# Performance work log

Measured on AMD Instinct MI355X. Metric: run time of the kernel, lower is better.

Reference implementation:

```python
import jax, jax.numpy as jnp
import numpy as np

B, TQ, TV, D, UNITS = 4, 256, 256, 512, 512
NEG_INF = -1e9

def setup_inputs() -> dict:
    key = jax.random.key(0)
    ks = jax.random.split(key, 5)
    return {
        "query": jax.random.normal(ks[0], (B, TQ, D), dtype=jnp.float32),
        "value": jax.random.normal(ks[1], (B, TV, D), dtype=jnp.float32),
        "mask": jnp.ones((B, TV), dtype=bool),
        "W1": jax.random.normal(ks[2], (D, UNITS), dtype=jnp.float32) * (1.0 / np.sqrt(D)),
        "W2": jax.random.normal(ks[3], (D, UNITS), dtype=jnp.float32) * (1.0 / np.sqrt(D)),
        "scale": jax.random.normal(ks[4], (UNITS,), dtype=jnp.float32),
    }

def reference(query, value, mask, W1, W2, scale):
    # Dual projections
    q = query @ W1                      # [B,Tq,U]
    k = value @ W2                      # [B,Tv,U]
    # Additive (Bahdanau) scores: sum(scale * tanh(q + k)) over units
    # broadcast tensor [B,Tq,Tv,U] is what the kernel would tile/fuse away
    t = jnp.tanh(q[:, :, None, :] + k[:, None, :, :])   # [B,Tq,Tv,U]
    scores = jnp.einsum('btvu,u->btv', t, scale)         # [B,Tq,Tv]
    # mask over value (key) positions
    scores = jnp.where(mask[:, None, :], scores, NEG_INF)
    attn = jax.nn.softmax(scores, axis=-1)               # [B,Tq,Tv]
    context = jnp.einsum('btv,bvd->btd', attn, value)    # [B,Tq,D]
    return context, attn
```

## Files before the change

### kernel.cpp

```cpp
#include <hip/hip_runtime.h>

typedef float f4 __attribute__((ext_vector_type(4)));
typedef float f2 __attribute__((ext_vector_type(2)));
typedef short short8 __attribute__((ext_vector_type(8)));
typedef float f32x4 __attribute__((ext_vector_type(4)));

#define NEG_INF -1e9f

__device__ inline void bsplit(float x, unsigned short& h, unsigned short& l) {
  union { float f; unsigned u; } a; a.f = x;
  unsigned rh = (a.u + 0x7fffu + ((a.u >> 16) & 1u)) >> 16;
  h = (unsigned short)rh;
  union { unsigned u; float f; } b; b.u = rh << 16;
  union { float f; unsigned u; } c; c.f = x - b.f;
  unsigned rl = (c.u + 0x7fffu + ((c.u >> 16) & 1u)) >> 16;
  l = (unsigned short)rl;
}

__device__ inline void gl_lds16(const void* g, void* l) {
  __builtin_amdgcn_global_load_lds(
      (const __attribute__((address_space(1))) unsigned int*)g,
      (__attribute__((address_space(3))) unsigned int*)l, 16, 0, 0);
}

__global__ __launch_bounds__(256) void conv_aw(
    const float* __restrict__ q, const float* __restrict__ v,
    const float* __restrict__ W1, const float* __restrict__ W2,
    unsigned short* __restrict__ Ahi, unsigned short* __restrict__ Alo,
    unsigned short* __restrict__ Whi, unsigned short* __restrict__ Wlo)
{
  __shared__ float ldsW[128][64];
  const int t = threadIdx.x;

  if (blockIdx.x < 512) {
    const int g = blockIdx.x * 256 + t;
    const int row64 = g & 63;
    const int panel = (g >> 6) & 31;
    const int kc    = g >> 11;
    const int rowg  = panel * 64 + row64;
    const float* src = (rowg < 1024) ? (q + (size_t)rowg * 512 + kc * 8)
                                     : (v + (size_t)(rowg - 1024) * 512 + kc * 8);
    f4 x0 = *reinterpret_cast<const f4*>(src);
    f4 x1 = *reinterpret_cast<const f4*>(src + 4);
    unsigned short h[8], l[8];
#pragma unroll
    for (int j = 0; j < 4; ++j) { bsplit(x0[j], h[j], l[j]); bsplit(x1[j], h[4+j], l[4+j]); }
    const size_t off = ((size_t)(panel * 64 + kc) * 64 + row64) * 8;
    short8 ph, pl;
#pragma unroll
    for (int j = 0; j < 8; ++j) { ph[j] = (short)h[j]; pl[j] = (short)l[j]; }
    *reinterpret_cast<short8*>(&Ahi[off]) = ph;
    *reinterpret_cast<short8*>(&Alo[off]) = pl;
    return;
  }

  const int bid   = blockIdx.x - 512;
  const int kslab = bid & 3;
  const int np    = (bid >> 2) & 7;
  const int z     = bid >> 5;
  const float* __restrict__ W = z ? W2 : W1;
  const int k0 = kslab * 128, n0 = np * 64;

#pragma unroll
  for (int it = 0; it < 8; ++it) {
    const int idx = it * 256 + t;
    const int kr  = idx >> 4;
    const int nc4 = (idx & 15) * 4;
    *reinterpret_cast<f4*>(&ldsW[kr][nc4]) =
        *reinterpret_cast<const f4*>(&W[(size_t)(k0 + kr) * 512 + n0 + nc4]);
  }
  __syncthreads();

  const int wpanel = z * 8 + np;
  const int n = t & 63;
#pragma unroll
  for (int it = 0; it < 4; ++it) {
    const int kcl = it * 4 + (t >> 6);
    short8 ph, pl;
#pragma unroll
    for (int j = 0; j < 8; ++j) {
      unsigned short h, l;
      bsplit(ldsW[kcl * 8 + j][n], h, l);
      ph[j] = (short)h; pl[j] = (short)l;
    }
    const size_t off = ((size_t)(wpanel * 64 + kslab * 16 + kcl) * 64 + n) * 8;
    *reinterpret_cast<short8*>(&Whi[off]) = ph;
    *reinterpret_cast<short8*>(&Wlo[off]) = pl;
  }
}

__global__ __launch_bounds__(256) void projmm(
    const unsigned short* __restrict__ Ahi, const unsigned short* __restrict__ Alo,
    const unsigned short* __restrict__ Whi, const unsigned short* __restrict__ Wlo,
    float* __restrict__ EQ, float* __restrict__ EKT)
{
  const int nb = blockIdx.x, mb = blockIdx.y, z = blockIdx.z;
  const int t = threadIdx.x;
  const int l = t & 63;
  const int w = t >> 6;
  const int wr = w >> 1, wc = w & 1;

  __shared__ __align__(16) short Ast[2][2][2048];
  __shared__ __align__(16) short Bst[2][2][2048];
  __shared__ float ldsT[64][67];

  const unsigned short* abase_h = Ahi + (size_t)(z * 16 + mb) * 32768;
  const unsigned short* abase_l = Alo + (size_t)(z * 16 + mb) * 32768;
  const unsigned short* wbase_h = Whi + (size_t)(z * 8 + nb) * 32768;
  const unsigned short* wbase_l = Wlo + (size_t)(z * 8 + nb) * 32768;

  const int ldst = (t >> 6) * 512;
  const int gsrc = t * 8;

#define STAGE(buf, ks)                                                        \
  do {                                                                        \
    gl_lds16(abase_h + (ks) * 2048 + gsrc, &Ast[buf][0][ldst]);               \
    gl_lds16(abase_l + (ks) * 2048 + gsrc, &Ast[buf][1][ldst]);               \
    gl_lds16(wbase_h + (ks) * 2048 + gsrc, &Bst[buf][0][ldst]);               \
    gl_lds16(wbase_l + (ks) * 2048 + gsrc, &Bst[buf][1][ldst]);               \
  } while (0)

  f32x4 acc[2][2] = {};
  STAGE(0, 0);
  __syncthreads();

  int buf = 0;
  for (int ks = 0; ks < 16; ++ks) {
    if (ks < 15) STAGE(buf ^ 1, ks + 1);
    const int kgo = (l >> 4) * 1024;
    short8 ah[2], al[2], bh[2], bl[2];
#pragma unroll
    for (int i = 0; i < 2; ++i) {
      const int ro = (wr * 32 + i * 16 + (l & 15)) * 16;
      ah[i] = *reinterpret_cast<const short8*>((const char*)&Ast[buf][0][0] + kgo + ro);
      al[i] = *reinterpret_cast<const short8*>((const char*)&Ast[buf][1][0] + kgo + ro);
    }
#pragma unroll
    for (int j = 0; j < 2; ++j) {
      const int co = (wc * 32 + j * 16 + (l & 15)) * 16;
      bh[j] = *reinterpret_cast<const short8*>((const char*)&Bst[buf][0][0] + kgo + co);
      bl[j] = *reinterpret_cast<const short8*>((const char*)&Bst[buf][1][0] + kgo + co);
    }
#pragma unroll
    for (int i = 0; i < 2; ++i)
#pragma unroll
      for (int j = 0; j < 2; ++j) {
        acc[i][j] = __builtin_amdgcn_mfma_f32_16x16x32_bf16(ah[i], bh[j], acc[i][j], 0, 0, 0);
        acc[i][j] = __builtin_amdgcn_mfma_f32_16x16x32_bf16(ah[i], bl[j], acc[i][j], 0, 0, 0);
        acc[i][j] = __builtin_amdgcn_mfma_f32_16x16x32_bf16(al[i], bh[j], acc[i][j], 0, 0, 0);
      }
    __syncthreads();
    buf ^= 1;
  }

  if (z == 0) {
#pragma unroll
    for (int i = 0; i < 2; ++i)
#pragma unroll
      for (int j = 0; j < 2; ++j)
#pragma unroll
        for (int r = 0; r < 4; ++r) {
          const int row = mb * 64 + wr * 32 + i * 16 + (l >> 4) * 4 + r;
          const int col = nb * 64 + wc * 32 + j * 16 + (l & 15);
          EQ[(size_t)row * 512 + col] = __expf(2.0f * acc[i][j][r]);
        }
  } else {
#pragma unroll
    for (int i = 0; i < 2; ++i)
#pragma unroll
      for (int j = 0; j < 2; ++j)
#pragma unroll
        for (int r = 0; r < 4; ++r) {
          const int rl = wr * 32 + i * 16 + (l >> 4) * 4 + r;
          const int cl = wc * 32 + j * 16 + (l & 15);
          ldsT[rl][cl] = __expf(2.0f * acc[i][j][r]);
        }
    __syncthreads();
    const int b  = (mb * 64) >> 8;
    const int v0 = (mb * 64) & 255;
    const int vl = t & 63;
#pragma unroll
    for (int it = 0; it < 16; ++it) {
      const int ul = it * 4 + (t >> 6);
      EKT[(size_t)b * 131072 + (size_t)(nb * 64 + ul) * 256 + v0 + vl] = ldsT[vl][ul];
    }
  }
#undef STAGE
}

__global__ __launch_bounds__(1024) void bah_attn(
    const float* __restrict__ EQ, const float* __restrict__ EKT,
    const float* __restrict__ value, const int* __restrict__ mask,
    const float* __restrict__ scale,
    float* __restrict__ ctx_out, float* __restrict__ attn_out)
{
  const int blk = blockIdx.x;
  const int b  = (blk & 7) >> 1;
  const int tg = (blk >> 3) + ((blk & 1) << 5);
  const int tq0 = tg * 4;
  const int bq  = b * 256 + tq0;

  const int tid = threadIdx.x;
  const int v4  = tid & 63;
  const int uq  = tid >> 6;
  const int w   = tid >> 6;
  const int l   = tid & 63;

  __shared__ f4    eq4s[512];
  __shared__ float ss[512];
  __shared__ float wredM[4][4];
  __shared__ float wredS[4][4];
  __shared__ float sumS_lds;
  __shared__ float atT[256][4];
  __shared__ __align__(16) char uA[131072];
  float* const ubufF = (float*)uA;
  float* const partF = (float*)uA;
  float* const ctxpF = (float*)(uA + 65536);

  const float* __restrict__ ekb = EKT + (size_t)b * (512 * 256);
  const float* __restrict__ eqb = EQ + (size_t)bq * 512;

  const int u0 = uq * 32;
  float* const wbase = ubufF + uq * 2048;

  const int r   = w & 3;
  const int vg  = w >> 2;
  const int v   = vg * 64 + l;

#define STAGEW(bufp, s)                                                       \
  do {                                                                        \
    _Pragma("unroll")                                                         \
    for (int c_ = 0; c_ < 4; ++c_)                                            \
      gl_lds16(ekb + (size_t)(u0 + (s) * 4 + c_) * 256 + l * 4,               \
               wbase + (bufp) * 1024 + c_ * 256);                             \
  } while (0)

  STAGEW(0, 0);

  const bool mok = (mask[b * 256 + v] != 0);

  {
    const int h  = tid >> 9;
    const int u2 = tid & 511;
    f2 e;
    e[0] = eqb[(size_t)(2 * h) * 512 + u2];
    e[1] = eqb[(size_t)(2 * h + 1) * 512 + u2];
    *(reinterpret_cast<f2*>(&eq4s[u2]) + h) = e;
    if (h == 0) ss[u2] = scale[u2];
  }
  __syncthreads();

  if (w == 0) {
    float s = 0.f;
#pragma unroll
    for (int j = 0; j < 8; ++j) s += ss[l + 64 * j];
#pragma unroll
    for (int off = 32; off; off >>= 1) s += __shfl_xor(s, off);
    if (l == 0) sumS_lds = s;
  }

  f2 accp[4][2] = {};
  int bufi = 0;
#pragma unroll 1
  for (int s = 0; s < 8; ++s) {
    if (s < 7) {
      STAGEW(bufi ^ 1, s + 1);
      asm volatile("s_waitcnt vmcnt(4)" ::: "memory");
    } else {
      asm volatile("s_waitcnt vmcnt(0)" ::: "memory");
    }
    __builtin_amdgcn_sched_barrier(0);
    const float* bp = wbase + bufi * 1024;
#pragma unroll
    for (int cp = 0; cp < 2; ++cp) {
      const int uA_ = u0 + s * 4 + 2 * cp;
      const f4 ekA4 = *reinterpret_cast<const f4*>(bp + (2 * cp) * 256 + v4 * 4);
      const f4 ekB4 = *reinterpret_cast<const f4*>(bp + (2 * cp + 1) * 256 + v4 * 4);
      const f2 ekA[2] = {{ekA4[0], ekA4[1]}, {ekA4[2], ekA4[3]}};
      const f2 ekB[2] = {{ekB4[0], ekB4[1]}, {ekB4[2], ekB4[3]}};
      const f4 eqA = eq4s[uA_];
      const f4 eqB = eq4s[uA_ + 1];
      const f2 sp  = *reinterpret_cast<const f2*>(&ss[uA_]);
      const f2 sA2 = {sp[0], sp[0]};
      const f2 sB2 = {sp[1], sp[1]};
      const f2 one2 = {1.0f, 1.0f};
#pragma unroll
      for (int i = 0; i < 4; ++i) {
        const f2 eA2 = {eqA[i], eqA[i]};
        const f2 eB2 = {eqB[i], eqB[i]};
#pragma unroll
        for (int jh = 0; jh < 2; ++jh) {
          const f2 dA  = __builtin_elementwise_fma(eA2, ekA[jh], one2);
          const f2 dB  = __builtin_elementwise_fma(eB2, ekB[jh], one2);
          const f2 num = __builtin_elementwise_fma(sA2, dB, sB2 * dA);
          const f2 P   = dA * dB;
          f2 r_;
          r_[0] = __builtin_amdgcn_rcpf(P[0]);
          r_[1] = __builtin_amdgcn_rcpf(P[1]);
          accp[i][jh] = __builtin_elementwise_fma(num, r_, accp[i][jh]);
        }
      }
    }
    bufi ^= 1;
  }

#pragma unroll
  for (int i = 0; i < 4; ++i) {
    const f4 a4 = {accp[i][0][0], accp[i][0][1], accp[i][1][0], accp[i][1][1]};
    *reinterpret_cast<f4*>(partF + uq * 2048 + i * 256 + v4 * 4) = a4;
  }
  __syncthreads();

  float sc, ex;
  {
    float p = 0.f;
#pragma unroll
    for (int u2 = 0; u2 < 16; ++u2) p += partF[u2 * 2048 + r * 256 + v];
    sc = mok ? (sumS_lds - 2.0f * p) : NEG_INF;
    float m = sc;
#pragma unroll
    for (int off = 32; off; off >>= 1) m = fmaxf(m, __shfl_xor(m, off));
    if (l == 0) wredM[r][vg] = m;
  }
  __syncthreads();

  {
    const float m = fmaxf(fmaxf(wredM[r][0], wredM[r][1]),
                          fmaxf(wredM[r][2], wredM[r][3]));
    ex = __expf(sc - m);
    float sm = ex;
#pragma unroll
    for (int off = 32; off; off >>= 1) sm += __shfl_xor(sm, off);
    if (l == 0) wredS[r][vg] = sm;
  }
  __syncthreads();

  {
    const float denom = (wredS[r][0] + wredS[r][1]) + (wredS[r][2] + wredS[r][3]);
    const float a = ex * __builtin_amdgcn_rcpf(denom);
    atT[v][r] = a;
    attn_out[(size_t)(bq + r) * 256 + v] = a;
  }
  __syncthreads();

  const int vc8 = w & 7;
  const int dh  = w >> 3;
  const float* __restrict__ vb = value + (size_t)b * (256 * 512) + dh * 256;
  f4 g0 = {0,0,0,0}, g1 = {0,0,0,0}, g2 = {0,0,0,0}, g3 = {0,0,0,0};
#pragma unroll 4
  for (int v2 = 0; v2 < 32; ++v2) {
    const int vv = vc8 * 32 + v2;
    const f4 a4 = *reinterpret_cast<const f4*>(&atT[vv][0]);
    const f4 x  = *reinterpret_cast<const f4*>(&vb[(size_t)vv * 512 + l * 4]);
    g0 += a4[0] * x;
    g1 += a4[1] * x;
    g2 += a4[2] * x;
    g3 += a4[3] * x;
  }
  {
    float* const cp = ctxpF + vc8 * 2048 + dh * 256 + l * 4;
    *reinterpret_cast<f4*>(cp + 0 * 512) = g0;
    *reinterpret_cast<f4*>(cp + 1 * 512) = g1;
    *reinterpret_cast<f4*>(cp + 2 * 512) = g2;
    *reinterpret_cast<f4*>(cp + 3 * 512) = g3;
  }
  __syncthreads();

  {
    const int row = tid >> 8;
    const int d2  = (tid & 255) * 2;
    f2 s = {0.f, 0.f};
#pragma unroll
    for (int vc = 0; vc < 8; ++vc)
      s += *reinterpret_cast<const f2*>(ctxpF + vc * 2048 + row * 512 + d2);
    *reinterpret_cast<f2*>(&ctx_out[(size_t)(bq + row) * 512 + d2]) = s;
  }
#undef STAGEW
}

extern "C" void kernel_launch(void* const* d_in, const int* in_sizes, int n_in,
                              void* d_out, int out_size, void* d_ws, size_t ws_size,
                              hipStream_t stream) {
  const float* query = (const float*)d_in[0];
  const float* value = (const float*)d_in[1];
  const int*   mask  = (const int*)d_in[2];
  const float* W1    = (const float*)d_in[3];
  const float* W2    = (const float*)d_in[4];
  const float* scale = (const float*)d_in[5];

  char* ws = (char*)d_ws;
  float* EQ  = (float*)(ws);
  float* EKT = (float*)(ws + (2u << 20));
  unsigned short* Ahi = (unsigned short*)(ws + (4u << 20));
  unsigned short* Alo = (unsigned short*)(ws + (6u << 20));
  unsigned short* Whi = (unsigned short*)(ws + (8u << 20));
  unsigned short* Wlo = (unsigned short*)(ws + (9u << 20));

  float* ctx  = (float*)d_out;
  float* attn = ctx + 4 * 256 * 512;

  conv_aw<<<dim3(576), 256, 0, stream>>>(query, value, W1, W2, Ahi, Alo, Whi, Wlo);
  projmm<<<dim3(8, 16, 2), 256, 0, stream>>>(Ahi, Alo, Whi, Wlo, EQ, EKT);
  bah_attn<<<dim3(256), 1024, 0, stream>>>(EQ, EKT, value, mask, scale, ctx, attn);
}
```

Measured before the change: 46.76 us.

## Fuse conversion, projection and attention into one cooperative kernel with grid syncs

```diff
diff --git a/kernel.cpp b/kernel.cpp
--- a/kernel.cpp
+++ b/kernel.cpp
@@ -1,4 +1,7 @@
 #include <hip/hip_runtime.h>
+#include <hip/hip_cooperative_groups.h>
+
+namespace cg = cooperative_groups;
 
 typedef float f4 __attribute__((ext_vector_type(4)));
 typedef float f2 __attribute__((ext_vector_type(2)));
@@ -23,188 +26,18 @@
       (__attribute__((address_space(3))) unsigned int*)l, 16, 0, 0);
 }
 
-__global__ __launch_bounds__(256) void conv_aw(
-    const float* __restrict__ q, const float* __restrict__ v,
+__global__ __launch_bounds__(1024) void bah_fused(
+    const float* __restrict__ query, const float* __restrict__ value,
+    const int* __restrict__ mask,
     const float* __restrict__ W1, const float* __restrict__ W2,
+    const float* __restrict__ scale,
     unsigned short* __restrict__ Ahi, unsigned short* __restrict__ Alo,
-    unsigned short* __restrict__ Whi, unsigned short* __restrict__ Wlo)
-{
-  __shared__ float ldsW[128][64];
-  const int t = threadIdx.x;
-
-  if (blockIdx.x < 512) {
-    const int g = blockIdx.x * 256 + t;
-    const int row64 = g & 63;
-    const int panel = (g >> 6) & 31;
-    const int kc    = g >> 11;
-    const int rowg  = panel * 64 + row64;
-    const float* src = (rowg < 1024) ? (q + (size_t)rowg * 512 + kc * 8)
-                                     : (v + (size_t)(rowg - 1024) * 512 + kc * 8);
-    f4 x0 = *reinterpret_cast<const f4*>(src);
-    f4 x1 = *reinterpret_cast<const f4*>(src + 4);
-    unsigned short h[8], l[8];
-#pragma unroll
-    for (int j = 0; j < 4; ++j) { bsplit(x0[j], h[j], l[j]); bsplit(x1[j], h[4+j], l[4+j]); }
-    const size_t off = ((size_t)(panel * 64 + kc) * 64 + row64) * 8;
-    short8 ph, pl;
-#pragma unroll
-    for (int j = 0; j < 8; ++j) { ph[j] = (short)h[j]; pl[j] = (short)l[j]; }
-    *reinterpret_cast<short8*>(&Ahi[off]) = ph;
-    *reinterpret_cast<short8*>(&Alo[off]) = pl;
-    return;
-  }
-
-  const int bid   = blockIdx.x - 512;
-  const int kslab = bid & 3;
-  const int np    = (bid >> 2) & 7;
-  const int z     = bid >> 5;
-  const float* __restrict__ W = z ? W2 : W1;
-  const int k0 = kslab * 128, n0 = np * 64;
-
-#pragma unroll
-  for (int it = 0; it < 8; ++it) {
-    const int idx = it * 256 + t;
-    const int kr  = idx >> 4;
-    const int nc4 = (idx & 15) * 4;
-    *reinterpret_cast<f4*>(&ldsW[kr][nc4]) =
-        *reinterpret_cast<const f4*>(&W[(size_t)(k0 + kr) * 512 + n0 + nc4]);
-  }
-  __syncthreads();
-
-  const int wpanel = z * 8 + np;
-  const int n = t & 63;
-#pragma unroll
-  for (int it = 0; it < 4; ++it) {
-    const int kcl = it * 4 + (t >> 6);
-    short8 ph, pl;
-#pragma unroll
-    for (int j = 0; j < 8; ++j) {
-      unsigned short h, l;
-      bsplit(ldsW[kcl * 8 + j][n], h, l);
-      ph[j] = (short)h; pl[j] = (short)l;
-    }
-    const size_t off = ((size_t)(wpanel * 64 + kslab * 16 + kcl) * 64 + n) * 8;
-    *reinterpret_cast<short8*>(&Whi[off]) = ph;
-    *reinterpret_cast<short8*>(&Wlo[off]) = pl;
-  }
-}
-
-__global__ __launch_bounds__(256) void projmm(
-    const unsigned short* __restrict__ Ahi, const unsigned short* __restrict__ Alo,
-    const unsigned short* __restrict__ Whi, const unsigned short* __restrict__ Wlo,
-    float* __restrict__ EQ, float* __restrict__ EKT)
-{
-  const int nb = blockIdx.x, mb = blockIdx.y, z = blockIdx.z;
-  const int t = threadIdx.x;
-  const int l = t & 63;
-  const int w = t >> 6;
-  const int wr = w >> 1, wc = w & 1;
-
-  __shared__ __align__(16) short Ast[2][2][2048];
-  __shared__ __align__(16) short Bst[2][2][2048];
-  __shared__ float ldsT[64][67];
-
-  const unsigned short* abase_h = Ahi + (size_t)(z * 16 + mb) * 32768;
-  const unsigned short* abase_l = Alo + (size_t)(z * 16 + mb) * 32768;
-  const unsigned short* wbase_h = Whi + (size_t)(z * 8 + nb) * 32768;
-  const unsigned short* wbase_l = Wlo + (size_t)(z * 8 + nb) * 32768;
-
-  const int ldst = (t >> 6) * 512;
-  const int gsrc = t * 8;
-
-#define STAGE(buf, ks)                                                        \
-  do {                                                                        \
-    gl_lds16(abase_h + (ks) * 2048 + gsrc, &Ast[buf][0][ldst]);               \
-    gl_lds16(abase_l + (ks) * 2048 + gsrc, &Ast[buf][1][ldst]);               \
-    gl_lds16(wbase_h + (ks) * 2048 + gsrc, &Bst[buf][0][ldst]);               \
-    gl_lds16(wbase_l + (ks) * 2048 + gsrc, &Bst[buf][1][ldst]);               \
-  } while (0)
-
-  f32x4 acc[2][2] = {};
-  STAGE(0, 0);
-  __syncthreads();
-
-  int buf = 0;
-  for (int ks = 0; ks < 16; ++ks) {
-    if (ks < 15) STAGE(buf ^ 1, ks + 1);
-    const int kgo = (l >> 4) * 1024;
-    short8 ah[2], al[2], bh[2], bl[2];
-#pragma unroll
-    for (int i = 0; i < 2; ++i) {
-      const int ro = (wr * 32 + i * 16 + (l & 15)) * 16;
-      ah[i] = *reinterpret_cast<const short8*>((const char*)&Ast[buf][0][0] + kgo + ro);
-      al[i] = *reinterpret_cast<const short8*>((const char*)&Ast[buf][1][0] + kgo + ro);
-    }
-#pragma unroll
-    for (int j = 0; j < 2; ++j) {
-      const int co = (wc * 32 + j * 16 + (l & 15)) * 16;
-      bh[j] = *reinterpret_cast<const short8*>((const char*)&Bst[buf][0][0] + kgo + co);
-      bl[j] = *reinterpret_cast<const short8*>((const char*)&Bst[buf][1][0] + kgo + co);
-    }
-#pragma unroll
-    for (int i = 0; i < 2; ++i)
-#pragma unroll
-      for (int j = 0; j < 2; ++j) {
-        acc[i][j] = __builtin_amdgcn_mfma_f32_16x16x32_bf16(ah[i], bh[j], acc[i][j], 0, 0, 0);
-        acc[i][j] = __builtin_amdgcn_mfma_f32_16x16x32_bf16(ah[i], bl[j], acc[i][j], 0, 0, 0);
-        acc[i][j] = __builtin_amdgcn_mfma_f32_16x16x32_bf16(al[i], bh[j], acc[i][j], 0, 0, 0);
-      }
-    __syncthreads();
-    buf ^= 1;
-  }
-
-  if (z == 0) {
-#pragma unroll
-    for (int i = 0; i < 2; ++i)
-#pragma unroll
-      for (int j = 0; j < 2; ++j)
-#pragma unroll
-        for (int r = 0; r < 4; ++r) {
-          const int row = mb * 64 + wr * 32 + i * 16 + (l >> 4) * 4 + r;
-          const int col = nb * 64 + wc * 32 + j * 16 + (l & 15);
-          EQ[(size_t)row * 512 + col] = __expf(2.0f * acc[i][j][r]);
-        }
-  } else {
-#pragma unroll
-    for (int i = 0; i < 2; ++i)
-#pragma unroll
-      for (int j = 0; j < 2; ++j)
-#pragma unroll
-        for (int r = 0; r < 4; ++r) {
-          const int rl = wr * 32 + i * 16 + (l >> 4) * 4 + r;
-          const int cl = wc * 32 + j * 16 + (l & 15);
-          ldsT[rl][cl] = __expf(2.0f * acc[i][j][r]);
-        }
-    __syncthreads();
-    const int b  = (mb * 64) >> 8;
-    const int v0 = (mb * 64) & 255;
-    const int vl = t & 63;
-#pragma unroll
-    for (int it = 0; it < 16; ++it) {
-      const int ul = it * 4 + (t >> 6);
-      EKT[(size_t)b * 131072 + (size_t)(nb * 64 + ul) * 256 + v0 + vl] = ldsT[vl][ul];
-    }
-  }
-#undef STAGE
-}
-
-__global__ __launch_bounds__(1024) void bah_attn(
-    const float* __restrict__ EQ, const float* __restrict__ EKT,
-    const float* __restrict__ value, const int* __restrict__ mask,
-    const float* __restrict__ scale,
+    unsigned short* __restrict__ Whi, unsigned short* __restrict__ Wlo,
+    float* __restrict__ EQ, float* __restrict__ EKT,
     float* __restrict__ ctx_out, float* __restrict__ attn_out)
 {
   const int blk = blockIdx.x;
-  const int b  = (blk & 7) >> 1;
-  const int tg = (blk >> 3) + ((blk & 1) << 5);
-  const int tq0 = tg * 4;
-  const int bq  = b * 256 + tq0;
-
   const int tid = threadIdx.x;
-  const int v4  = tid & 63;
-  const int uq  = tid >> 6;
-  const int w   = tid >> 6;
-  const int l   = tid & 63;
 
   __shared__ f4    eq4s[512];
   __shared__ float ss[512];
@@ -213,169 +46,355 @@
   __shared__ float sumS_lds;
   __shared__ float atT[256][4];
   __shared__ __align__(16) char uA[131072];
-  float* const ubufF = (float*)uA;
-  float* const partF = (float*)uA;
-  float* const ctxpF = (float*)(uA + 65536);
-
-  const float* __restrict__ ekb = EKT + (size_t)b * (512 * 256);
-  const float* __restrict__ eqb = EQ + (size_t)bq * 512;
-
-  const int u0 = uq * 32;
-  float* const wbase = ubufF + uq * 2048;
-
-  const int r   = w & 3;
-  const int vg  = w >> 2;
-  const int v   = vg * 64 + l;
+
+  if (blk < 128) {
+    const int g = blk * 1024 + tid;
+    const int row64 = g & 63;
+    const int panel = (g >> 6) & 31;
+    const int kc    = g >> 11;
+    const int rowg  = panel * 64 + row64;
+    const float* src = (rowg < 1024) ? (query + (size_t)rowg * 512 + kc * 8)
+                                     : (value + (size_t)(rowg - 1024) * 512 + kc * 8);
+    f4 x0 = *reinterpret_cast<const f4*>(src);
+    f4 x1 = *reinterpret_cast<const f4*>(src + 4);
+    unsigned short h[8], lo[8];
+#pragma unroll
+    for (int j = 0; j < 4; ++j) { bsplit(x0[j], h[j], lo[j]); bsplit(x1[j], h[4+j], lo[4+j]); }
+    const size_t off = ((size_t)(panel * 64 + kc) * 64 + row64) * 8;
+    short8 ph, pl;
+#pragma unroll
+    for (int j = 0; j < 8; ++j) { ph[j] = (short)h[j]; pl[j] = (short)lo[j]; }
+    *reinterpret_cast<short8*>(&Ahi[off]) = ph;
+    *reinterpret_cast<short8*>(&Alo[off]) = pl;
+  } else if (blk < 144) {
+    const int bid = blk - 128;
+    const int np  = bid & 7;
+    const int z   = bid >> 3;
+    const int sg  = tid >> 8;
+    const int t   = tid & 255;
+    const float* __restrict__ W = z ? W2 : W1;
+    const int k0 = sg * 128, n0 = np * 64;
+    float* const ldsW = (float*)(uA + sg * 32768);
+
+#pragma unroll
+    for (int it = 0; it < 8; ++it) {
+      const int idx = it * 256 + t;
+      const int kr  = idx >> 4;
+      const int nc4 = (idx & 15) * 4;
+      *reinterpret_cast<f4*>(ldsW + kr * 64 + nc4) =
+          *reinterpret_cast<const f4*>(&W[(size_t)(k0 + kr) * 512 + n0 + nc4]);
+    }
+    __syncthreads();
+
+    const int wpanel = z * 8 + np;
+    const int n = t & 63;
+#pragma unroll
+    for (int it = 0; it < 4; ++it) {
+      const int kcl = it * 4 + (t >> 6);
+      short8 ph, pl;
+#pragma unroll
+      for (int j = 0; j < 8; ++j) {
+        unsigned short h, lo;
+        bsplit(ldsW[(kcl * 8 + j) * 64 + n], h, lo);
+        ph[j] = (short)h; pl[j] = (short)lo;
+      }
+      const size_t off = ((size_t)(wpanel * 64 + sg * 16 + kcl) * 64 + n) * 8;
+      *reinterpret_cast<short8*>(&Whi[off]) = ph;
+      *reinterpret_cast<short8*>(&Wlo[off]) = pl;
+    }
+  }
+
+  cg::this_grid().sync();
+
+  {
+    const int nb = blk & 7, mb = (blk >> 3) & 15, z = blk >> 7;
+    const int sg = tid >> 8;
+    const int t  = tid & 255;
+    const int l  = t & 63;
+    const int w4 = t >> 6;
+    const int wr = w4 >> 1, wc = w4 & 1;
+
+    const unsigned short* abase_h = Ahi + (size_t)(z * 16 + mb) * 32768;
+    const unsigned short* abase_l = Alo + (size_t)(z * 16 + mb) * 32768;
+    const unsigned short* wbase_h = Whi + (size_t)(z * 8 + nb) * 32768;
+    const unsigned short* wbase_l = Wlo + (size_t)(z * 8 + nb) * 32768;
+
+    char* const sgbase = uA + sg * 32768;
+    const int gsrc = t * 8;
+    const int ldso = (t >> 6) * 1024;
+
+#define CHA(buf, hl) (sgbase + ((buf) * 2 + (hl)) * 4096)
+#define CHB(buf, hl) (sgbase + 16384 + ((buf) * 2 + (hl)) * 4096)
+#define PSTAGE(buf, ksg)                                                      \
+    do {                                                                      \
+      gl_lds16(abase_h + (ksg) * 2048 + gsrc, CHA(buf, 0) + ldso);            \
+      gl_lds16(abase_l + (ksg) * 2048 + gsrc, CHA(buf, 1) + ldso);            \
+      gl_lds16(wbase_h + (ksg) * 2048 + gsrc, CHB(buf, 0) + ldso);            \
+      gl_lds16(wbase_l + (ksg) * 2048 + gsrc, CHB(buf, 1) + ldso);            \
+    } while (0)
+
+    f32x4 acc[2][2] = {};
+    PSTAGE(0, sg * 4);
+    __syncthreads();
+
+    int buf = 0;
+#pragma unroll 1
+    for (int kl = 0; kl < 4; ++kl) {
+      if (kl < 3) PSTAGE(buf ^ 1, sg * 4 + kl + 1);
+      const int kgo = (l >> 4) * 1024;
+      short8 ah[2], al[2], bh[2], bl[2];
+#pragma unroll
+      for (int i = 0; i < 2; ++i) {
+        const int ro = (wr * 32 + i * 16 + (l & 15)) * 16;
+        ah[i] = *reinterpret_cast<const short8*>(CHA(buf, 0) + kgo + ro);
+        al[i] = *reinterpret_cast<const short8*>(CHA(buf, 1) + kgo + ro);
+      }
+#pragma unroll
+      for (int j = 0; j < 2; ++j) {
+        const int co = (wc * 32 + j * 16 + (l & 15)) * 16;
+        bh[j] = *reinterpret_cast<const short8*>(CHB(buf, 0) + kgo + co);
+        bl[j] = *reinterpret_cast<const short8*>(CHB(buf, 1) + kgo + co);
+      }
+#pragma unroll
+      for (int i = 0; i < 2; ++i)
+#pragma unroll
+        for (int j = 0; j < 2; ++j) {
+          acc[i][j] = __builtin_amdgcn_mfma_f32_16x16x32_bf16(ah[i], bh[j], acc[i][j], 0, 0, 0);
+          acc[i][j] = __builtin_amdgcn_mfma_f32_16x16x32_bf16(ah[i], bl[j], acc[i][j], 0, 0, 0);
+          acc[i][j] = __builtin_amdgcn_mfma_f32_16x16x32_bf16(al[i], bh[j], acc[i][j], 0, 0, 0);
+        }
+      __syncthreads();
+      buf ^= 1;
+    }
+
+    float* const red = (float*)uA;
+#pragma unroll
+    for (int i = 0; i < 2; ++i)
+#pragma unroll
+      for (int j = 0; j < 2; ++j)
+        *reinterpret_cast<f32x4*>(&red[((size_t)sg * 256 + t) * 16 + (i * 2 + j) * 4]) = acc[i][j];
+    __syncthreads();
+
+    const int t2 = tid >> 2;
+    const int fi = tid & 3;
+    const int i2 = fi >> 1, j2 = fi & 1;
+    const int base = t2 * 16 + fi * 4;
+    const f4 s0 = *reinterpret_cast<const f4*>(&red[0 * 4096 + base]);
+    const f4 s1 = *reinterpret_cast<const f4*>(&red[1 * 4096 + base]);
+    const f4 s2 = *reinterpret_cast<const f4*>(&red[2 * 4096 + base]);
+    const f4 s3 = *reinterpret_cast<const f4*>(&red[3 * 4096 + base]);
+    const f4 rs = (s0 + s1) + (s2 + s3);
+
+    const int l2  = t2 & 63;
+    const int w42 = t2 >> 6;
+    const int wr2 = w42 >> 1, wc2 = w42 & 1;
+    const int row_local = wr2 * 32 + i2 * 16 + (l2 >> 4) * 4;
+    const int col_local = wc2 * 32 + j2 * 16 + (l2 & 15);
+
+    if (z == 0) {
+#pragma unroll
+      for (int r = 0; r < 4; ++r)
+        EQ[(size_t)(mb * 64 + row_local + r) * 512 + nb * 64 + col_local] =
+            __expf(2.0f * rs[r]);
+    } else {
+      float* const ldsT = (float*)(uA + 65536);
+      __syncthreads();
+#pragma unroll
+      for (int r = 0; r < 4; ++r)
+        ldsT[(row_local + r) * 67 + col_local] = __expf(2.0f * rs[r]);
+      __syncthreads();
+      const int bb = (mb * 64) >> 8;
+      const int v0 = (mb * 64) & 255;
+      const int vl = tid & 63;
+#pragma unroll
+      for (int it2 = 0; it2 < 4; ++it2) {
+        const int ul = it2 * 16 + (tid >> 6);
+        EKT[(size_t)bb * 131072 + (size_t)(nb * 64 + ul) * 256 + v0 + vl] =
+            ldsT[vl * 67 + ul];
+      }
+    }
+#undef PSTAGE
+#undef CHA
+#undef CHB
+  }
+
+  cg::this_grid().sync();
+
+  {
+    const int b  = (blk & 7) >> 1;
+    const int tg = (blk >> 3) + ((blk & 1) << 5);
+    const int tq0 = tg * 4;
+    const int bq  = b * 256 + tq0;
+
+    const int v4  = tid & 63;
+    const int uq  = tid >> 6;
+    const int w   = tid >> 6;
+    const int l   = tid & 63;
+
+    float* const ubufF = (float*)uA;
+    float* const partF = (float*)uA;
+    float* const ctxpF = (float*)(uA + 65536);
+
+    const float* __restrict__ ekb = EKT + (size_t)b * (512 * 256);
+    const float* __restrict__ eqb = EQ + (size_t)bq * 512;
+
+    const int u0 = uq * 32;
+    float* const wbase = ubufF + uq * 2048;
+
+    const int r   = w & 3;
+    const int vg  = w >> 2;
+    const int v   = vg * 64 + l;
 
 #define STAGEW(bufp, s)                                                       \
-  do {                                                                        \
-    _Pragma("unroll")                                                         \
-    for (int c_ = 0; c_ < 4; ++c_)                                            \
-      gl_lds16(ekb + (size_t)(u0 + (s) * 4 + c_) * 256 + l * 4,               \
-               wbase + (bufp) * 1024 + c_ * 256);                             \
-  } while (0)
-
-  STAGEW(0, 0);
-
-  const bool mok = (mask[b * 256 + v] != 0);
-
-  {
-    const int h  = tid >> 9;
-    const int u2 = tid & 511;
-    f2 e;
-    e[0] = eqb[(size_t)(2 * h) * 512 + u2];
-    e[1] = eqb[(size_t)(2 * h + 1) * 512 + u2];
-    *(reinterpret_cast<f2*>(&eq4s[u2]) + h) = e;
-    if (h == 0) ss[u2] = scale[u2];
+    do {                                                                      \
+      _Pragma("unroll")                                                       \
+      for (int c_ = 0; c_ < 4; ++c_)                                          \
+        gl_lds16(ekb + (size_t)(u0 + (s) * 4 + c_) * 256 + l * 4,             \
+                 wbase + (bufp) * 1024 + c_ * 256);                           \
+    } while (0)
+
+    STAGEW(0, 0);
+
+    const bool mok = (mask[b * 256 + v] != 0);
+
+    {
+      const int h  = tid >> 9;
+      const int u2 = tid & 511;
+      f2 e;
+      e[0] = eqb[(size_t)(2 * h) * 512 + u2];
+      e[1] = eqb[(size_t)(2 * h + 1) * 512 + u2];
+      *(reinterpret_cast<f2*>(&eq4s[u2]) + h) = e;
+      if (h == 0) ss[u2] = scale[u2];
+    }
+    __syncthreads();
+
+    if (w == 0) {
+      float s = 0.f;
+#pragma unroll
+      for (int j = 0; j < 8; ++j) s += ss[l + 64 * j];
+#pragma unroll
+      for (int off = 32; off; off >>= 1) s += __shfl_xor(s, off);
+      if (l == 0) sumS_lds = s;
+    }
+
+    f2 accp[4][2] = {};
+    int bufi = 0;
+#pragma unroll 1
+    for (int s = 0; s < 8; ++s) {
+      if (s < 7) {
+        STAGEW(bufi ^ 1, s + 1);
+        asm volatile("s_waitcnt vmcnt(4)" ::: "memory");
+      } else {
+        asm volatile("s_waitcnt vmcnt(0)" ::: "memory");
+      }
+      __builtin_amdgcn_sched_barrier(0);
+      const float* bp = wbase + bufi * 1024;
+#pragma unroll
+      for (int cp = 0; cp < 2; ++cp) {
+        const int uA_ = u0 + s * 4 + 2 * cp;
+        const f4 ekA4 = *reinterpret_cast<const f4*>(bp + (2 * cp) * 256 + v4 * 4);
+        const f4 ekB4 = *reinterpret_cast<const f4*>(bp + (2 * cp + 1) * 256 + v4 * 4);
+        const f2 ekA[2] = {{ekA4[0], ekA4[1]}, {ekA4[2], ekA4[3]}};
+        const f2 ekB[2] = {{ekB4[0], ekB4[1]}, {ekB4[2], ekB4[3]}};
+        const f4 eqA = eq4s[uA_];
+        const f4 eqB = eq4s[uA_ + 1];
+        const f2 sp  = *reinterpret_cast<const f2*>(&ss[uA_]);
+        const f2 sA2 = {sp[0], sp[0]};
+        const f2 sB2 = {sp[1], sp[1]};
+        const f2 one2 = {1.0f, 1.0f};
+#pragma unroll
+        for (int i = 0; i < 4; ++i) {
+          const f2 eA2 = {eqA[i], eqA[i]};
+          const f2 eB2 = {eqB[i], eqB[i]};
+#pragma unroll
+          for (int jh = 0; jh < 2; ++jh) {
+            const f2 dA  = __builtin_elementwise_fma(eA2, ekA[jh], one2);
+            const f2 dB  = __builtin_elementwise_fma(eB2, ekB[jh], one2);
+            const f2 num = __builtin_elementwise_fma(sA2, dB, sB2 * dA);
+            const f2 P   = dA * dB;
+            f2 r_;
+            r_[0] = __builtin_amdgcn_rcpf(P[0]);
+            r_[1] = __builtin_amdgcn_rcpf(P[1]);
+            accp[i][jh] = __builtin_elementwise_fma(num, r_, accp[i][jh]);
+          }
+        }
+      }
+      bufi ^= 1;
+    }
+
+#pragma unroll
+    for (int i = 0; i < 4; ++i) {
+      const f4 a4 = {accp[i][0][0], accp[i][0][1], accp[i][1][0], accp[i][1][1]};
+      *reinterpret_cast<f4*>(partF + uq * 2048 + i * 256 + v4 * 4) = a4;
+    }
+    __syncthreads();
+
+    float sc, ex;
+    {
+      float p = 0.f;
+#pragma unroll
+      for (int u2 = 0; u2 < 16; ++u2) p += partF[u2 * 2048 + r * 256 + v];
+      sc = mok ? (sumS_lds - 2.0f * p) : NEG_INF;
+      float m = sc;
+#pragma unroll
+      for (int off = 32; off; off >>= 1) m = fmaxf(m, __shfl_xor(m, off));
+      if (l == 0) wredM[r][vg] = m;
+    }
+    __syncthreads();
+
+    {
+      const float m = fmaxf(fmaxf(wredM[r][0], wredM[r][1]),
+                            fmaxf(wredM[r][2], wredM[r][3]));
+      ex = __expf(sc - m);
+      float sm = ex;
+#pragma unroll
+      for (int off = 32; off; off >>= 1) sm += __shfl_xor(sm, off);
+      if (l == 0) wredS[r][vg] = sm;
+    }
+    __syncthreads();
+
+    {
+      const float denom = (wredS[r][0] + wredS[r][1]) + (wredS[r][2] + wredS[r][3]);
+      const float a = ex * __builtin_amdgcn_rcpf(denom);
+      atT[v][r] = a;
+      attn_out[(size_t)(bq + r) * 256 + v] = a;
+    }
+    __syncthreads();
+
+    const int vc8 = w & 7;
+    const int dh  = w >> 3;
+    const float* __restrict__ vb = value + (size_t)b * (256 * 512) + dh * 256;
+    f4 g0 = {0,0,0,0}, g1 = {0,0,0,0}, g2 = {0,0,0,0}, g3 = {0,0,0,0};
+#pragma unroll 4
+    for (int v2 = 0; v2 < 32; ++v2) {
+      const int vv = vc8 * 32 + v2;
+      const f4 a4 = *reinterpret_cast<const f4*>(&atT[vv][0]);
+      const f4 x  = *reinterpret_cast<const f4*>(&vb[(size_t)vv * 512 + l * 4]);
+      g0 += a4[0] * x;
+      g1 += a4[1] * x;
+      g2 += a4[2] * x;
+      g3 += a4[3] * x;
+    }
+    {
+      float* const cp = ctxpF + vc8 * 2048 + dh * 256 + l * 4;
+      *reinterpret_cast<f4*>(cp + 0 * 512) = g0;
+      *reinterpret_cast<f4*>(cp + 1 * 512) = g1;
+      *reinterpret_cast<f4*>(cp + 2 * 512) = g2;
+      *reinterpret_cast<f4*>(cp + 3 * 512) = g3;
+    }
+    __syncthreads();
+
+    {
+      const int row = tid >> 8;
+      const int d2  = (tid & 255) * 2;
+      f2 s = {0.f, 0.f};
+#pragma unroll
+      for (int vc = 0; vc < 8; ++vc)
+        s += *reinterpret_cast<const f2*>(ctxpF + vc * 2048 + row * 512 + d2);
+      *reinterpret_cast<f2*>(&ctx_out[(size_t)(bq + row) * 512 + d2]) = s;
+    }
+#undef STAGEW
   }
-  __syncthreads();
-
-  if (w == 0) {
-    float s = 0.f;
-#pragma unroll
-    for (int j = 0; j < 8; ++j) s += ss[l + 64 * j];
-#pragma unroll
-    for (int off = 32; off; off >>= 1) s += __shfl_xor(s, off);
-    if (l == 0) sumS_lds = s;
-  }
-
-  f2 accp[4][2] = {};
-  int bufi = 0;
-#pragma unroll 1
-  for (int s = 0; s < 8; ++s) {
-    if (s < 7) {
-      STAGEW(bufi ^ 1, s + 1);
-      asm volatile("s_waitcnt vmcnt(4)" ::: "memory");
-    } else {
-      asm volatile("s_waitcnt vmcnt(0)" ::: "memory");
-    }
-    __builtin_amdgcn_sched_barrier(0);
-    const float* bp = wbase + bufi * 1024;
-#pragma unroll
-    for (int cp = 0; cp < 2; ++cp) {
-      const int uA_ = u0 + s * 4 + 2 * cp;
-      const f4 ekA4 = *reinterpret_cast<const f4*>(bp + (2 * cp) * 256 + v4 * 4);
-      const f4 ekB4 = *reinterpret_cast<const f4*>(bp + (2 * cp + 1) * 256 + v4 * 4);
-      const f2 ekA[2] = {{ekA4[0], ekA4[1]}, {ekA4[2], ekA4[3]}};
-      const f2 ekB[2] = {{ekB4[0], ekB4[1]}, {ekB4[2], ekB4[3]}};
-      const f4 eqA = eq4s[uA_];
-      const f4 eqB = eq4s[uA_ + 1];
-      const f2 sp  = *reinterpret_cast<const f2*>(&ss[uA_]);
-      const f2 sA2 = {sp[0], sp[0]};
-      const f2 sB2 = {sp[1], sp[1]};
-      const f2 one2 = {1.0f, 1.0f};
-#pragma unroll
-      for (int i = 0; i < 4; ++i) {
-        const f2 eA2 = {eqA[i], eqA[i]};
-        const f2 eB2 = {eqB[i], eqB[i]};
-#pragma unroll
-        for (int jh = 0; jh < 2; ++jh) {
-          const f2 dA  = __builtin_elementwise_fma(eA2, ekA[jh], one2);
-          const f2 dB  = __builtin_elementwise_fma(eB2, ekB[jh], one2);
-          const f2 num = __builtin_elementwise_fma(sA2, dB, sB2 * dA);
-          const f2 P   = dA * dB;
-          f2 r_;
-          r_[0] = __builtin_amdgcn_rcpf(P[0]);
-          r_[1] = __builtin_amdgcn_rcpf(P[1]);
-          accp[i][jh] = __builtin_elementwise_fma(num, r_, accp[i][jh]);
-        }
-      }
-    }
-    bufi ^= 1;
-  }
-
-#pragma unroll
-  for (int i = 0; i < 4; ++i) {
-    const f4 a4 = {accp[i][0][0], accp[i][0][1], accp[i][1][0], accp[i][1][1]};
-    *reinterpret_cast<f4*>(partF + uq * 2048 + i * 256 + v4 * 4) = a4;
-  }
-  __syncthreads();
-
-  float sc, ex;
-  {
-    float p = 0.f;
-#pragma unroll
-    for (int u2 = 0; u2 < 16; ++u2) p += partF[u2 * 2048 + r * 256 + v];
-    sc = mok ? (sumS_lds - 2.0f * p) : NEG_INF;
-    float m = sc;
-#pragma unroll
-    for (int off = 32; off; off >>= 1) m = fmaxf(m, __shfl_xor(m, off));
-    if (l == 0) wredM[r][vg] = m;
-  }
-  __syncthreads();
-
-  {
-    const float m = fmaxf(fmaxf(wredM[r][0], wredM[r][1]),
-                          fmaxf(wredM[r][2], wredM[r][3]));
-    ex = __expf(sc - m);
-    float sm = ex;
-#pragma unroll
-    for (int off = 32; off; off >>= 1) sm += __shfl_xor(sm, off);
-    if (l == 0) wredS[r][vg] = sm;
-  }
-  __syncthreads();
-
-  {
-    const float denom = (wredS[r][0] + wredS[r][1]) + (wredS[r][2] + wredS[r][3]);
-    const float a = ex * __builtin_amdgcn_rcpf(denom);
-    atT[v][r] = a;
-    attn_out[(size_t)(bq + r) * 256 + v] = a;
-  }
-  __syncthreads();
-
-  const int vc8 = w & 7;
-  const int dh  = w >> 3;
-  const float* __restrict__ vb = value + (size_t)b * (256 * 512) + dh * 256;
-  f4 g0 = {0,0,0,0}, g1 = {0,0,0,0}, g2 = {0,0,0,0}, g3 = {0,0,0,0};
-#pragma unroll 4
-  for (int v2 = 0; v2 < 32; ++v2) {
-    const int vv = vc8 * 32 + v2;
-    const f4 a4 = *reinterpret_cast<const f4*>(&atT[vv][0]);
-    const f4 x  = *reinterpret_cast<const f4*>(&vb[(size_t)vv * 512 + l * 4]);
-    g0 += a4[0] * x;
-    g1 += a4[1] * x;
-    g2 += a4[2] * x;
-    g3 += a4[3] * x;
-  }
-  {
-    float* const cp = ctxpF + vc8 * 2048 + dh * 256 + l * 4;
-    *reinterpret_cast<f4*>(cp + 0 * 512) = g0;
-    *reinterpret_cast<f4*>(cp + 1 * 512) = g1;
-    *reinterpret_cast<f4*>(cp + 2 * 512) = g2;
-    *reinterpret_cast<f4*>(cp + 3 * 512) = g3;
-  }
-  __syncthreads();
-
-  {
-    const int row = tid >> 8;
-    const int d2  = (tid & 255) * 2;
-    f2 s = {0.f, 0.f};
-#pragma unroll
-    for (int vc = 0; vc < 8; ++vc)
-      s += *reinterpret_cast<const f2*>(ctxpF + vc * 2048 + row * 512 + d2);
-    *reinterpret_cast<f2*>(&ctx_out[(size_t)(bq + row) * 512 + d2]) = s;
-  }
-#undef STAGEW
 }
 
 extern "C" void kernel_launch(void* const* d_in, const int* in_sizes, int n_in,
@@ -399,7 +418,11 @@
   float* ctx  = (float*)d_out;
   float* attn = ctx + 4 * 256 * 512;
 
-  conv_aw<<<dim3(576), 256, 0, stream>>>(query, value, W1, W2, Ahi, Alo, Whi, Wlo);
-  projmm<<<dim3(8, 16, 2), 256, 0, stream>>>(Ahi, Alo, Whi, Wlo, EQ, EKT);
-  bah_attn<<<dim3(256), 1024, 0, stream>>>(EQ, EKT, value, mask, scale, ctx, attn);
+  void* args[] = {
+    (void*)&query, (void*)&value, (void*)&mask, (void*)&W1, (void*)&W2,
+    (void*)&scale, (void*)&Ahi, (void*)&Alo, (void*)&Whi, (void*)&Wlo,
+    (void*)&EQ, (void*)&EKT, (void*)&ctx, (void*)&attn
+  };
+  hipLaunchCooperativeKernel((const void*)bah_fused, dim3(256), dim3(1024),
+                             args, 0, stream);
 }
```

After: 120.9 us. +158.5%, slower.

## Split projection GEMM K loop across two thread groups with LDS reduction

Applied to the files above, without the earlier changes.

```diff
diff --git a/kernel.cpp b/kernel.cpp
--- a/kernel.cpp
+++ b/kernel.cpp
@@ -89,19 +89,22 @@
   }
 }
 
-__global__ __launch_bounds__(256) void projmm(
+__global__ __launch_bounds__(512) void projmm(
     const unsigned short* __restrict__ Ahi, const unsigned short* __restrict__ Alo,
     const unsigned short* __restrict__ Whi, const unsigned short* __restrict__ Wlo,
     float* __restrict__ EQ, float* __restrict__ EKT)
 {
   const int nb = blockIdx.x, mb = blockIdx.y, z = blockIdx.z;
-  const int t = threadIdx.x;
-  const int l = t & 63;
-  const int w = t >> 6;
+  const int tid = threadIdx.x;
+  const int sg = tid >> 8;
+  const int t  = tid & 255;
+  const int l  = t & 63;
+  const int w  = t >> 6;
   const int wr = w >> 1, wc = w & 1;
 
-  __shared__ __align__(16) short Ast[2][2][2048];
-  __shared__ __align__(16) short Bst[2][2][2048];
+  __shared__ __align__(16) short Ast[2][2][2][2048];
+  __shared__ __align__(16) short Bst[2][2][2][2048];
+  __shared__ __align__(16) f32x4 red4[4][256];
   __shared__ float ldsT[64][67];
 
   const unsigned short* abase_h = Ahi + (size_t)(z * 16 + mb) * 32768;
@@ -109,37 +112,39 @@
   const unsigned short* wbase_h = Whi + (size_t)(z * 8 + nb) * 32768;
   const unsigned short* wbase_l = Wlo + (size_t)(z * 8 + nb) * 32768;
 
-  const int ldst = (t >> 6) * 512;
+  const int ldst = w * 512;
   const int gsrc = t * 8;
 
 #define STAGE(buf, ks)                                                        \
   do {                                                                        \
-    gl_lds16(abase_h + (ks) * 2048 + gsrc, &Ast[buf][0][ldst]);               \
-    gl_lds16(abase_l + (ks) * 2048 + gsrc, &Ast[buf][1][ldst]);               \
-    gl_lds16(wbase_h + (ks) * 2048 + gsrc, &Bst[buf][0][ldst]);               \
-    gl_lds16(wbase_l + (ks) * 2048 + gsrc, &Bst[buf][1][ldst]);               \
+    gl_lds16(abase_h + (ks) * 2048 + gsrc, &Ast[sg][buf][0][ldst]);           \
+    gl_lds16(abase_l + (ks) * 2048 + gsrc, &Ast[sg][buf][1][ldst]);           \
+    gl_lds16(wbase_h + (ks) * 2048 + gsrc, &Bst[sg][buf][0][ldst]);           \
+    gl_lds16(wbase_l + (ks) * 2048 + gsrc, &Bst[sg][buf][1][ldst]);           \
   } while (0)
 
   f32x4 acc[2][2] = {};
-  STAGE(0, 0);
+  const int ks0 = sg * 8;
+  STAGE(0, ks0);
   __syncthreads();
 
   int buf = 0;
-  for (int ks = 0; ks < 16; ++ks) {
-    if (ks < 15) STAGE(buf ^ 1, ks + 1);
+#pragma unroll 1
+  for (int kl = 0; kl < 8; ++kl) {
+    if (kl < 7) STAGE(buf ^ 1, ks0 + kl + 1);
     const int kgo = (l >> 4) * 1024;
     short8 ah[2], al[2], bh[2], bl[2];
 #pragma unroll
     for (int i = 0; i < 2; ++i) {
       const int ro = (wr * 32 + i * 16 + (l & 15)) * 16;
-      ah[i] = *reinterpret_cast<const short8*>((const char*)&Ast[buf][0][0] + kgo + ro);
-      al[i] = *reinterpret_cast<const short8*>((const char*)&Ast[buf][1][0] + kgo + ro);
+      ah[i] = *reinterpret_cast<const short8*>((const char*)&Ast[sg][buf][0][0] + kgo + ro);
+      al[i] = *reinterpret_cast<const short8*>((const char*)&Ast[sg][buf][1][0] + kgo + ro);
     }
 #pragma unroll
     for (int j = 0; j < 2; ++j) {
       const int co = (wc * 32 + j * 16 + (l & 15)) * 16;
-      bh[j] = *reinterpret_cast<const short8*>((const char*)&Bst[buf][0][0] + kgo + co);
-      bl[j] = *reinterpret_cast<const short8*>((const char*)&Bst[buf][1][0] + kgo + co);
+      bh[j] = *reinterpret_cast<const short8*>((const char*)&Bst[sg][buf][0][0] + kgo + co);
+      bl[j] = *reinterpret_cast<const short8*>((const char*)&Bst[sg][buf][1][0] + kgo + co);
     }
 #pragma unroll
     for (int i = 0; i < 2; ++i)
@@ -153,35 +158,54 @@
     buf ^= 1;
   }
 
+  if (sg == 1) {
+#pragma unroll
+    for (int i = 0; i < 2; ++i)
+#pragma unroll
+      for (int j = 0; j < 2; ++j)
+        red4[i * 2 + j][t] = acc[i][j];
+  }
+  __syncthreads();
+
   if (z == 0) {
-#pragma unroll
-    for (int i = 0; i < 2; ++i)
-#pragma unroll
-      for (int j = 0; j < 2; ++j)
-#pragma unroll
-        for (int r = 0; r < 4; ++r) {
-          const int row = mb * 64 + wr * 32 + i * 16 + (l >> 4) * 4 + r;
-          const int col = nb * 64 + wc * 32 + j * 16 + (l & 15);
-          EQ[(size_t)row * 512 + col] = __expf(2.0f * acc[i][j][r]);
+    if (sg == 0) {
+#pragma unroll
+      for (int i = 0; i < 2; ++i)
+#pragma unroll
+        for (int j = 0; j < 2; ++j) {
+          const f32x4 o = red4[i * 2 + j][t];
+          const f32x4 s = acc[i][j] + o;
+#pragma unroll
+          for (int r = 0; r < 4; ++r) {
+            const int row = mb * 64 + wr * 32 + i * 16 + (l >> 4) * 4 + r;
+            const int col = nb * 64 + wc * 32 + j * 16 + (l & 15);
+            EQ[(size_t)row * 512 + col] = __expf(2.0f * s[r]);
+          }
         }
+    }
   } else {
-#pragma unroll
-    for (int i = 0; i < 2; ++i)
-#pragma unroll
-      for (int j = 0; j < 2; ++j)
-#pragma unroll
-        for (int r = 0; r < 4; ++r) {
-          const int rl = wr * 32 + i * 16 + (l >> 4) * 4 + r;
-          const int cl = wc * 32 + j * 16 + (l & 15);
-          ldsT[rl][cl] = __expf(2.0f * acc[i][j][r]);
+    if (sg == 0) {
+#pragma unroll
+      for (int i = 0; i < 2; ++i)
+#pragma unroll
+        for (int j = 0; j < 2; ++j) {
+          const f32x4 o = red4[i * 2 + j][t];
+          const f32x4 s = acc[i][j] + o;
+#pragma unroll
+          for (int r = 0; r < 4; ++r) {
+            const int rl = wr * 32 + i * 16 + (l >> 4) * 4 + r;
+            const int cl = wc * 32 + j * 16 + (l & 15);
+            ldsT[rl][cl] = __expf(2.0f * s[r]);
+          }
         }
+    }
     __syncthreads();
     const int b  = (mb * 64) >> 8;
     const int v0 = (mb * 64) & 255;
-    const int vl = t & 63;
-#pragma unroll
-    for (int it = 0; it < 16; ++it) {
-      const int ul = it * 4 + (t >> 6);
+    const int vl = tid & 63;
+#pragma unroll
+    for (int it = 0; it < 8; ++it) {
+      const int ul = it * 8 + (tid >> 6);
       EKT[(size_t)b * 131072 + (size_t)(nb * 64 + ul) * 256 + v0 + vl] = ldsT[vl][ul];
     }
   }
@@ -400,6 +424,6 @@
   float* attn = ctx + 4 * 256 * 512;
 
   conv_aw<<<dim3(576), 256, 0, stream>>>(query, value, W1, W2, Ahi, Alo, Whi, Wlo);
-  projmm<<<dim3(8, 16, 2), 256, 0, stream>>>(Ahi, Alo, Whi, Wlo, EQ, EKT);
+  projmm<<<dim3(8, 16, 2), 512, 0, stream>>>(Ahi, Alo, Whi, Wlo, EQ, EKT);
   bah_attn<<<dim3(256), 1024, 0, stream>>>(EQ, EKT, value, mask, scale, ctx, attn);
 }
```

New measurement: 42.81 us. 8.5% less time.
